# Performance work log

Measured on AMD Instinct MI355X. Metric: run time of the kernel, lower is better.

The kernel has to match this reference:

```python
import jax, jax.numpy as jnp
import numpy as np

N, C, H, W = 8, 64, 56, 56
NL_C = 0.5
EPS = 1e-5


def _bn(x, gamma, beta, mean, var):
    # eval-mode BatchNorm2d over channel dim of NCHW
    inv = jax.lax.rsqrt(var + EPS)
    return (x - mean[:, None, None]) * (inv * gamma)[:, None, None] + beta[:, None, None]


def setup_inputs() -> dict:
    key = jax.random.key(0)
    ks = jax.random.split(key, 11)
    l = jax.random.normal(ks[0], (N, C, H, W), jnp.float32)
    w_inside = jax.random.normal(ks[1], (C, C, 1, 1), jnp.float32) * 0.1  # 1x1 conv, OIHW
    gamma1 = jax.random.normal(ks[2], (C,), jnp.float32)
    beta1 = jax.random.normal(ks[3], (C,), jnp.float32)
    mean1 = jax.random.normal(ks[4], (C,), jnp.float32)
    var1 = jax.random.uniform(ks[5], (C,), jnp.float32, 0.5, 1.5)
    w_dw = jax.random.normal(ks[6], (C, 1, 3, 3), jnp.float32) * 0.1  # depthwise 3x3
    gamma2 = jax.random.normal(ks[7], (C,), jnp.float32)
    beta2 = jax.random.normal(ks[8], (C,), jnp.float32)
    mean2 = jax.random.normal(ks[9], (C,), jnp.float32)
    var2 = jax.random.uniform(ks[10], (C,), jnp.float32, 0.5, 1.5)
    return dict(l=l, w_inside=w_inside, gamma1=gamma1, beta1=beta1, mean1=mean1,
                var1=var1, w_dw=w_dw, gamma2=gamma2, beta2=beta2, mean2=mean2, var2=var2)


def reference(l, w_inside, gamma1, beta1, mean1, var1, w_dw, gamma2, beta2, mean2, var2):
    n, n_in, h, w = l.shape
    c_red = int(NL_C * n_in)  # channels used for theta/phi

    # conv_inside: 1x1 conv (no bias) + BN + relu6 -> g
    g = jax.lax.conv_general_dilated(l, w_inside, (1, 1), 'VALID',
                                     dimension_numbers=('NCHW', 'OIHW', 'NCHW'))
    g = jnp.clip(_bn(g, gamma1, beta1, mean1, var1), 0.0, 6.0)

    theta = l[:, :c_red]  # == phi in the original code
    # f: [N, H, W, H, W]
    f = jnp.einsum('niab,nicd->nabcd', theta, theta)
    # softmax over flattened (a,b) then over flattened (c,d)
    f = jax.nn.softmax(f.reshape(n, h * w, h, w), axis=1)
    f = jax.nn.softmax(f.reshape(n, h * w, h * w), axis=2)
    f = f.reshape(n, h, w, h, w)

    out = jnp.einsum('nabcd,nicd->niab', f, g)
    out = out / h * w  # (f / H) * W as in the original

    # depthwise 3x3 conv, pad 1, no bias
    out = jax.lax.conv_general_dilated(out, w_dw, (1, 1), ((1, 1), (1, 1)),
                                       dimension_numbers=('NCHW', 'OIHW', 'NCHW'),
                                       feature_group_count=n_in)
    out = _bn(out, gamma2, beta2, mean2, var2)
    return out + l
```

## Files before the change

kernel.cpp:

```cpp
#include <hip/hip_runtime.h>

#define HW   3136
#define NCH  64
#define CRED 32
#define NB   8
#define EPSV 1e-5f
#define QS2  7

#define SQRT_L2E 1.2011224087f
#define LOG2_L2E 0.5287663729f

typedef __attribute__((ext_vector_type(8))) short short8;
typedef __attribute__((ext_vector_type(4))) float f32x4;
typedef __attribute__((ext_vector_type(2))) float f32x2;
typedef _Float16 half_t;
typedef __attribute__((ext_vector_type(2))) _Float16 half2v;
typedef __attribute__((ext_vector_type(4))) _Float16 half4v;

#define MFMA_B16 __builtin_amdgcn_mfma_f32_16x16x32_bf16

__device__ __forceinline__ unsigned short f2b(float x) {
    union { float f; unsigned u; } v; v.f = x;
    unsigned r = v.u + 0x7fff + ((v.u >> 16) & 1);
    return (unsigned short)(r >> 16);
}

__device__ __forceinline__ float ex2(float x) {
#if __has_builtin(__builtin_amdgcn_exp2f)
    return __builtin_amdgcn_exp2f(x);
#else
    float r;
    asm volatile("v_exp_f32 %0, %1" : "=v"(r) : "v"(x));
    return r;
#endif
}

__device__ __forceinline__ unsigned cvtpk(float a, float b) {
    unsigned r;
    asm("v_cvt_pk_bf16_f32 %0, %1, %2" : "=v"(r) : "v"(a), "v"(b));
    return r;
}

__global__ __launch_bounds__(256) void k1_conv1x1(
    const float* __restrict__ l, const float* __restrict__ w,
    const float* __restrict__ gamma, const float* __restrict__ beta,
    const float* __restrict__ mean, const float* __restrict__ var,
    unsigned short* __restrict__ theta_bf, unsigned short* __restrict__ Gbt)
{
    __shared__ float Wt[NCH][65];
    __shared__ float Lt[NCH][65];
    const int t  = threadIdx.x;
    const int n  = blockIdx.y;
    const int p0 = blockIdx.x * 64;

    for (int idx = t; idx < NCH * 64; idx += 256) {
        int c = idx >> 6, j = idx & 63;
        Wt[c][j] = w[j * NCH + c];
        Lt[c][j] = l[((size_t)n * NCH + c) * HW + p0 + j];
    }
    __syncthreads();

    {
        const int p = t >> 2, c0 = (t & 3) * 8;
        unsigned short pk[8];
#pragma unroll
        for (int j = 0; j < 8; ++j) pk[j] = f2b(Lt[c0 + j][p] * SQRT_L2E);
        *(short8*)&theta_bf[((size_t)n * HW + p0 + p) * CRED + c0] = *(short8*)pk;
    }

    const int i   = t & 63;
    const int pj0 = t >> 6;
    const float mu = mean[i];
    const float sc = rsqrtf(var[i] + EPSV) * gamma[i];
    const float bi = beta[i];

    float acc[16];
#pragma unroll
    for (int k = 0; k < 16; ++k) acc[k] = 0.f;
#pragma unroll
    for (int c = 0; c < NCH; ++c) {
        float wci = Wt[c][i];
#pragma unroll
        for (int k = 0; k < 16; ++k) acc[k] += wci * Lt[c][pj0 + 4 * k];
    }
    __syncthreads();

#pragma unroll
    for (int k = 0; k < 16; ++k) {
        float y = (acc[k] - mu) * sc + bi;
        y = fminf(fmaxf(y, 0.f), 6.f);
        Wt[i][pj0 + 4 * k] = y;
    }
    __syncthreads();

    {
        const int ir = t >> 2, pc = (t & 3) * 16;
        unsigned short pk[16];
#pragma unroll
        for (int j = 0; j < 16; ++j) pk[j] = f2b(Wt[ir][pc + j]);
        unsigned short* dst = &Gbt[((size_t)n * NCH + ir) * HW + p0 + pc];
        *(short8*)&dst[0] = *(short8*)&pk[0];
        *(short8*)&dst[8] = *(short8*)&pk[8];
    }
}

__global__ __launch_bounds__(256) void k2s_stats(
    const unsigned short* __restrict__ theta_bf, float* __restrict__ zpart)
{
    const int t = threadIdx.x, w = t >> 6, lane = t & 63;
    const int lo = lane & 15, hi = lane >> 4;
    const int n = blockIdx.z, psp = blockIdx.y;
    const int q0 = blockIdx.x * 64;

    const unsigned short* thn = theta_bf + (size_t)n * HW * CRED;

    const short8 afrag = *(const short8*)&thn[(q0 + w * 16 + lo) * CRED + hi * 8];

    float z[4] = {0.f, 0.f, 0.f, 0.f};

    short8 bf[4];
    {
        const int p0 = psp * 448;
#pragma unroll
        for (int ss = 0; ss < 4; ++ss)
            bf[ss] = *(const short8*)&thn[(p0 + ss * 16 + lo) * CRED + hi * 8];
    }

    for (int pt = 0; pt < 7; ++pt) {
        const int pn = psp * 448 + ((pt < 6) ? (pt + 1) * 64 : 6 * 64);
        short8 nf[4];
#pragma unroll
        for (int ss = 0; ss < 4; ++ss)
            nf[ss] = *(const short8*)&thn[(pn + ss * 16 + lo) * CRED + hi * 8];

#pragma unroll
        for (int ss = 0; ss < 4; ++ss) {
            f32x4 zero = {0.f, 0.f, 0.f, 0.f};
            f32x4 d = MFMA_B16(afrag, bf[ss], zero, 0, 0, 0);
#pragma unroll
            for (int r = 0; r < 4; ++r) z[r] += ex2(d[r]);
        }

#pragma unroll
        for (int ss = 0; ss < 4; ++ss) bf[ss] = nf[ss];
    }

#pragma unroll
    for (int r = 0; r < 4; ++r) {
        float v = z[r];
        v += __shfl_xor(v, 1, 64);
        v += __shfl_xor(v, 2, 64);
        v += __shfl_xor(v, 4, 64);
        v += __shfl_xor(v, 8, 64);
        z[r] = v;
    }
    if (lo == 0) {
        f32x4 st = {z[0], z[1], z[2], z[3]};
        *(f32x4*)&zpart[((size_t)psp * NB + n) * HW + q0 + w * 16 + hi * 4] = st;
    }
}

__global__ __launch_bounds__(256) void k2c_combine(
    const float* __restrict__ zpart, float* __restrict__ crow)
{
    const int idx = blockIdx.x * 256 + threadIdx.x;
    float s = 0.f;
#pragma unroll
    for (int ps = 0; ps < QS2; ++ps) s += zpart[(size_t)ps * NB * HW + idx];
    crow[idx] = LOG2_L2E - __log2f(s);
}

__global__ __launch_bounds__(256) void k3f_fused(
    const unsigned short* __restrict__ theta_bf,
    const unsigned short* __restrict__ Gbt,
    const float* __restrict__ crow,
    half_t* __restrict__ Part, float* __restrict__ Zpart)
{
    __shared__ unsigned short Glt[64][76];
    __shared__ unsigned short El[64][76];

    const int t = threadIdx.x, w = t >> 6, lane = t & 63;
    const int lo = lane & 15, hi = lane >> 4;
    const int n = blockIdx.z, qsp = blockIdx.y;
    const int pblk = blockIdx.x * 64;
    const int pw = w * 16;

    const unsigned short* thn = theta_bf + (size_t)n * HW * CRED;
    const float* crn = crow + (size_t)n * HW;

    const short8 bp = *(const short8*)&thn[(pblk + pw + lo) * CRED + hi * 8];

    f32x4 acc[4];
#pragma unroll
    for (int it = 0; it < 4; ++it) acc[it] = (f32x4){0.f, 0.f, 0.f, 0.f};
    float zl = 0.f;

    for (int tile = 0; tile < 7; ++tile) {
        const int qb = qsp * 448 + tile * 64;
        __syncthreads();
        {
            const int ir = t >> 2, qoff = (t & 3) * 16;
            const unsigned short* src = &Gbt[((size_t)n * NCH + ir) * HW + qb + qoff];
            *(short8*)&Glt[ir][qoff]     = *(const short8*)&src[0];
            *(short8*)&Glt[ir][qoff + 8] = *(const short8*)&src[8];
        }
        short8 aqr[4];
        f32x4  cvr[4];
#pragma unroll
        for (int s = 0; s < 4; ++s) {
            aqr[s] = *(const short8*)&thn[(qb + s * 16 + lo) * CRED + hi * 8];
            cvr[s] = *(const f32x4*)&crn[qb + s * 16 + hi * 4];
        }
        __syncthreads();

#pragma unroll
        for (int s = 0; s < 4; ++s) {
            f32x4 d = MFMA_B16(aqr[s], bp, cvr[s], 0, 0, 0);
            float e0 = ex2(ex2(d[0]));
            float e1 = ex2(ex2(d[1]));
            float e2 = ex2(ex2(d[2]));
            float e3 = ex2(ex2(d[3]));
            zl += (e0 + e1) + (e2 + e3);
            unsigned* dst = (unsigned*)&El[pw + lo][s * 16 + hi * 4];
            dst[0] = cvtpk(e0, e1);
            dst[1] = cvtpk(e2, e3);
        }

#pragma unroll
        for (int ks = 0; ks < 2; ++ks) {
            const short8 ae = *(const short8*)&El[pw + lo][ks * 32 + hi * 8];
#pragma unroll
            for (int it = 0; it < 4; ++it) {
                const short8 bg = *(const short8*)&Glt[it * 16 + lo][ks * 32 + hi * 8];
                acc[it] = MFMA_B16(ae, bg, acc[it], 0, 0, 0);
            }
        }
    }

    half_t* Pn = Part + ((size_t)n * QS2 + qsp) * (size_t)NCH * HW;
#pragma unroll
    for (int it = 0; it < 4; ++it) {
        half4v h;
        h[0] = (half_t)acc[it][0]; h[1] = (half_t)acc[it][1];
        h[2] = (half_t)acc[it][2]; h[3] = (half_t)acc[it][3];
        *(half4v*)&Pn[(size_t)(it * 16 + lo) * HW + pblk + pw + hi * 4] = h;
    }
    zl += __shfl_xor(zl, 16, 64);
    zl += __shfl_xor(zl, 32, 64);
    if (lane < 16)
        Zpart[((size_t)n * QS2 + qsp) * HW + pblk + pw + lane] = zl;
}

__global__ __launch_bounds__(256) void k34_reduce_dw(
    const half_t* __restrict__ Part, const float* __restrict__ Zpart,
    const float* __restrict__ l, const float* __restrict__ wdw,
    const float* __restrict__ gamma, const float* __restrict__ beta,
    const float* __restrict__ mean, const float* __restrict__ var,
    float* __restrict__ out)
{
    __shared__ float op[4][16][56];
    __shared__ float zsh[16 * 56];
    __shared__ float wsh[36];

    const int t    = threadIdx.x;
    const int band = blockIdx.x;
    const int i0   = blockIdx.y * 4;
    const int n    = blockIdx.z;
    const int y0   = band * 14;

    if (t < 36) wsh[t] = wdw[i0 * 9 + t];

    for (int idx = t; idx < 16 * 56; idx += 256) {
        const int yy = y0 - 1 + idx / 56, x = idx % 56;
        if (yy >= 0 && yy < 56) {
            const int p = yy * 56 + x;
            float z = 0.f;
#pragma unroll
            for (int qs = 0; qs < QS2; ++qs)
                z += Zpart[((size_t)n * QS2 + qs) * HW + p];
            zsh[idx] = 1.f / z;
        }
    }
    __syncthreads();

    for (int idx = t; idx < 4 * 16 * 56; idx += 256) {
        const int c = idx / (16 * 56), rem = idx % (16 * 56);
        const int yy = y0 - 1 + rem / 56, x = rem % 56;
        if (yy >= 0 && yy < 56) {
            const int p = yy * 56 + x;
            const int i = i0 + c;
            float s = 0.f;
#pragma unroll
            for (int qs = 0; qs < QS2; ++qs)
                s += (float)Part[(((size_t)n * QS2 + qs) * NCH + i) * HW + p];
            op[c][rem / 56][x] = s * zsh[rem];
        }
    }
    __syncthreads();

    for (int idx = t; idx < 4 * 14 * 56; idx += 256) {
        const int c = idx / (14 * 56), rem = idx % (14 * 56);
        const int y = y0 + rem / 56, x = rem % 56;
        const int i = i0 + c;

        float acc = 0.f;
#pragma unroll
        for (int dy = -1; dy <= 1; ++dy) {
            const int yy = y + dy;
            if (yy < 0 || yy >= 56) continue;
            const int ly = yy - (y0 - 1);
#pragma unroll
            for (int dx = -1; dx <= 1; ++dx) {
                const int xx = x + dx;
                if (xx < 0 || xx >= 56) continue;
                acc += wsh[c * 9 + (dy + 1) * 3 + (dx + 1)] * op[c][ly][xx];
            }
        }
        const float sc = rsqrtf(var[i] + EPSV) * gamma[i];
        const size_t e = ((size_t)n * NCH + i) * HW + y * 56 + x;
        out[e] = (acc - mean[i]) * sc + beta[i] + l[e];
    }
}

extern "C" void kernel_launch(void* const* d_in, const int* in_sizes, int n_in,
                              void* d_out, int out_size, void* d_ws, size_t ws_size,
                              hipStream_t stream)
{
    const float* l      = (const float*)d_in[0];
    const float* w_in   = (const float*)d_in[1];
    const float* gamma1 = (const float*)d_in[2];
    const float* beta1  = (const float*)d_in[3];
    const float* mean1  = (const float*)d_in[4];
    const float* var1   = (const float*)d_in[5];
    const float* w_dw   = (const float*)d_in[6];
    const float* gamma2 = (const float*)d_in[7];
    const float* beta2  = (const float*)d_in[8];
    const float* mean2  = (const float*)d_in[9];
    const float* var2   = (const float*)d_in[10];
    float* out = (float*)d_out;

    char* ws = (char*)d_ws;
    const size_t szTheta = (size_t)NB * HW * CRED * 2;
    const size_t szGbt   = (size_t)NB * NCH * HW * 2;
    const size_t szCrow  = (size_t)NB * HW * 4;
    const size_t szZpt   = (size_t)QS2 * NB * HW * 4;
    const size_t szZp    = (size_t)NB * QS2 * HW * 4;

    unsigned short* theta_bf = (unsigned short*)ws;
    unsigned short* Gbt      = (unsigned short*)(ws + szTheta);
    float* crow   = (float*)(ws + szTheta + szGbt);
    float* zpart  = (float*)(ws + szTheta + szGbt + szCrow);
    float* Zp     = (float*)(ws + szTheta + szGbt + szCrow + szZpt);
    half_t* Part  = (half_t*)(ws + szTheta + szGbt + szCrow + szZpt + szZp);
    (void)ws_size;

    k1_conv1x1<<<dim3(HW / 64, NB), 256, 0, stream>>>(
        l, w_in, gamma1, beta1, mean1, var1, theta_bf, Gbt);

    k2s_stats<<<dim3(HW / 64, QS2, NB), 256, 0, stream>>>(theta_bf, zpart);

    k2c_combine<<<dim3((NB * HW) / 256), 256, 0, stream>>>(zpart, crow);

    k3f_fused<<<dim3(HW / 64, QS2, NB), 256, 0, stream>>>(
        theta_bf, Gbt, crow, Part, Zp);

    k34_reduce_dw<<<dim3(4, NCH / 4, NB), 256, 0, stream>>>(
        Part, Zp, l, w_dw, gamma2, beta2, mean2, var2, out);
}
```

Measured before the change: 104.9 us.

## Exploit symmetry of theta Gram matrix to halve softmax stats computation

The first-softmax column sums are now computed only over upper-triangular 64x64 tile pairs of the symmetric theta·theta matrix. Each off-diagonal tile contributes its exp sums to both row and column totals through atomicAdd into a zeroed accumulator. This removes the per-split partial buffer and the reduction over splits, and replaces them with a memset plus many float atomics. The grid is now 1225 blocks of one tile each, and the triangular index is recovered with a serial while loop. Atomic contention and the loss of the old prefetch pipeline may offset the halved MFMA and exp2 work.

```diff
diff --git a/kernel.cpp b/kernel.cpp
--- a/kernel.cpp
+++ b/kernel.cpp
@@ -6,6 +6,8 @@
 #define NB   8
 #define EPSV 1e-5f
 #define QS2  7
+#define NTB  49
+#define NTRI (NTB * (NTB + 1) / 2)
 
 #define SQRT_L2E 1.2011224087f
 #define LOG2_L2E 0.5287663729f
@@ -104,70 +106,56 @@
     }
 }
 
-__global__ __launch_bounds__(256) void k2s_stats(
-    const unsigned short* __restrict__ theta_bf, float* __restrict__ zpart)
+__global__ __launch_bounds__(256) void k2s_tri(
+    const unsigned short* __restrict__ theta_bf, float* __restrict__ zacc)
 {
     const int t = threadIdx.x, w = t >> 6, lane = t & 63;
     const int lo = lane & 15, hi = lane >> 4;
-    const int n = blockIdx.z, psp = blockIdx.y;
-    const int q0 = blockIdx.x * 64;
+    const int n = blockIdx.z;
+
+    int r = blockIdx.x, a = 0;
+    while (r >= NTB - a) { r -= NTB - a; ++a; }
+    const int b = a + r;
 
     const unsigned short* thn = theta_bf + (size_t)n * HW * CRED;
-
-    const short8 afrag = *(const short8*)&thn[(q0 + w * 16 + lo) * CRED + hi * 8];
-
-    float z[4] = {0.f, 0.f, 0.f, 0.f};
-
-    short8 bf[4];
-    {
-        const int p0 = psp * 448;
-#pragma unroll
-        for (int ss = 0; ss < 4; ++ss)
-            bf[ss] = *(const short8*)&thn[(p0 + ss * 16 + lo) * CRED + hi * 8];
-    }
-
-    for (int pt = 0; pt < 7; ++pt) {
-        const int pn = psp * 448 + ((pt < 6) ? (pt + 1) * 64 : 6 * 64);
-        short8 nf[4];
-#pragma unroll
-        for (int ss = 0; ss < 4; ++ss)
-            nf[ss] = *(const short8*)&thn[(pn + ss * 16 + lo) * CRED + hi * 8];
-
-#pragma unroll
-        for (int ss = 0; ss < 4; ++ss) {
-            f32x4 zero = {0.f, 0.f, 0.f, 0.f};
-            f32x4 d = MFMA_B16(afrag, bf[ss], zero, 0, 0, 0);
-#pragma unroll
-            for (int r = 0; r < 4; ++r) z[r] += ex2(d[r]);
-        }
-
-#pragma unroll
-        for (int ss = 0; ss < 4; ++ss) bf[ss] = nf[ss];
-    }
-
-#pragma unroll
-    for (int r = 0; r < 4; ++r) {
-        float v = z[r];
+    float* zn = zacc + (size_t)n * HW;
+
+    const short8 afrag =
+        *(const short8*)&thn[(a * 64 + w * 16 + lo) * CRED + hi * 8];
+
+    float zq[4] = {0.f, 0.f, 0.f, 0.f};
+#pragma unroll
+    for (int ss = 0; ss < 4; ++ss) {
+        const short8 bfrag =
+            *(const short8*)&thn[(b * 64 + ss * 16 + lo) * CRED + hi * 8];
+        f32x4 zero = {0.f, 0.f, 0.f, 0.f};
+        f32x4 d = MFMA_B16(afrag, bfrag, zero, 0, 0, 0);
+        float e0 = ex2(d[0]), e1 = ex2(d[1]), e2 = ex2(d[2]), e3 = ex2(d[3]);
+        zq[0] += e0; zq[1] += e1; zq[2] += e2; zq[3] += e3;
+        if (a != b) {
+            float c = (e0 + e1) + (e2 + e3);
+            c += __shfl_xor(c, 16, 64);
+            c += __shfl_xor(c, 32, 64);
+            if (hi == 0) atomicAdd(&zn[b * 64 + ss * 16 + lo], c);
+        }
+    }
+
+#pragma unroll
+    for (int rr = 0; rr < 4; ++rr) {
+        float v = zq[rr];
         v += __shfl_xor(v, 1, 64);
         v += __shfl_xor(v, 2, 64);
         v += __shfl_xor(v, 4, 64);
         v += __shfl_xor(v, 8, 64);
-        z[r] = v;
-    }
-    if (lo == 0) {
-        f32x4 st = {z[0], z[1], z[2], z[3]};
-        *(f32x4*)&zpart[((size_t)psp * NB + n) * HW + q0 + w * 16 + hi * 4] = st;
+        if (lo == 0) atomicAdd(&zn[a * 64 + w * 16 + hi * 4 + rr], v);
     }
 }
 
 __global__ __launch_bounds__(256) void k2c_combine(
-    const float* __restrict__ zpart, float* __restrict__ crow)
+    const float* __restrict__ zacc, float* __restrict__ crow)
 {
     const int idx = blockIdx.x * 256 + threadIdx.x;
-    float s = 0.f;
-#pragma unroll
-    for (int ps = 0; ps < QS2; ++ps) s += zpart[(size_t)ps * NB * HW + idx];
-    crow[idx] = LOG2_L2E - __log2f(s);
+    crow[idx] = LOG2_L2E - __log2f(zacc[idx]);
 }
 
 __global__ __launch_bounds__(256) void k3f_fused(
@@ -343,23 +331,25 @@
     const size_t szTheta = (size_t)NB * HW * CRED * 2;
     const size_t szGbt   = (size_t)NB * NCH * HW * 2;
     const size_t szCrow  = (size_t)NB * HW * 4;
-    const size_t szZpt   = (size_t)QS2 * NB * HW * 4;
+    const size_t szZacc  = (size_t)QS2 * NB * HW * 4;
     const size_t szZp    = (size_t)NB * QS2 * HW * 4;
 
     unsigned short* theta_bf = (unsigned short*)ws;
     unsigned short* Gbt      = (unsigned short*)(ws + szTheta);
     float* crow   = (float*)(ws + szTheta + szGbt);
-    float* zpart  = (float*)(ws + szTheta + szGbt + szCrow);
-    float* Zp     = (float*)(ws + szTheta + szGbt + szCrow + szZpt);
-    half_t* Part  = (half_t*)(ws + szTheta + szGbt + szCrow + szZpt + szZp);
+    float* zacc   = (float*)(ws + szTheta + szGbt + szCrow);
+    float* Zp     = (float*)(ws + szTheta + szGbt + szCrow + szZacc);
+    half_t* Part  = (half_t*)(ws + szTheta + szGbt + szCrow + szZacc + szZp);
     (void)ws_size;
+
+    hipMemsetAsync(zacc, 0, (size_t)NB * HW * 4, stream);
 
     k1_conv1x1<<<dim3(HW / 64, NB), 256, 0, stream>>>(
         l, w_in, gamma1, beta1, mean1, var1, theta_bf, Gbt);
 
-    k2s_stats<<<dim3(HW / 64, QS2, NB), 256, 0, stream>>>(theta_bf, zpart);
-
-    k2c_combine<<<dim3((NB * HW) / 256), 256, 0, stream>>>(zpart, crow);
+    k2s_tri<<<dim3(NTRI, 1, NB), 256, 0, stream>>>(theta_bf, zacc);
+
+    k2c_combine<<<dim3((NB * HW) / 256), 256, 0, stream>>>(zacc, crow);
 
     k3f_fused<<<dim3(HW / 64, QS2, NB), 256, 0, stream>>>(
         theta_bf, Gbt, crow, Part, Zp);
```

After: 121.3 us. 15.7% more time.
